# Performance work log

Hardware: AMD Instinct MI355X
Metric: run time of the kernel (lower is better)

## Reference

```python
import jax, jax.numpy as jnp
import numpy as np

N = 50000      # nodes
E = 1200000    # edges (before self loops)
IN = 128       # in_channels
HID = 32       # hidden_channels
HEADS = 2
HC = HID * HEADS  # 64, per-layer output channels
OUT = 40       # classes
NEG_SLOPE = 0.2
BN_EPS = 1e-5


def setup_inputs() -> dict:
    key = jax.random.key(0)
    ks = jax.random.split(key, 20)
    def nrm(k, shape, scale=0.1):
        return jax.random.normal(k, shape, dtype=jnp.float32) * scale
    return {
        "x": jax.random.normal(ks[0], (N, IN), dtype=jnp.float32),
        "edge_index": jax.random.randint(ks[1], (2, E), 0, N),
        "W1": nrm(ks[2], (IN, HC)),
        "a_src1": nrm(ks[3], (HEADS, HID)),
        "a_dst1": nrm(ks[4], (HEADS, HID)),
        "b1": nrm(ks[5], (HC,)),
        "bn_gamma": 1.0 + nrm(ks[6], (HC,)),
        "bn_beta": nrm(ks[7], (HC,)),
        "bn_mean": nrm(ks[8], (HC,)),
        "bn_var": jax.random.uniform(ks[9], (HC,), minval=0.5, maxval=1.5),
        "W2": nrm(ks[10], (HC, HC)),
        "a_src2": nrm(ks[11], (HEADS, HID)),
        "a_dst2": nrm(ks[12], (HEADS, HID)),
        "b2": nrm(ks[13], (HC,)),
        "Wf": nrm(ks[14], (HC, OUT)),
        "bf": nrm(ks[15], (OUT,)),
    }


def _gat_conv(x, src, dst, W, a_s, a_d, b):
    # x: [N, F_in] -> h: [N, H, C]
    h = (x @ W).reshape(N, HEADS, HID)
    alpha_src = jnp.einsum("nhc,hc->nh", h, a_s)  # [N, H]
    alpha_dst = jnp.einsum("nhc,hc->nh", h, a_d)  # [N, H]
    e = alpha_src[src] + alpha_dst[dst]            # [E, H]
    e = jnp.where(e > 0, e, NEG_SLOPE * e)         # leaky_relu(0.2)
    # scatter softmax over edges grouped by dst node
    m = jax.ops.segment_max(e, dst, num_segments=N)
    m = jnp.where(jnp.isfinite(m), m, 0.0)         # isolated nodes -> -inf fill
    ee = jnp.exp(e - m[dst])
    denom = jax.ops.segment_sum(ee, dst, num_segments=N)
    alpha = ee / (denom[dst] + 1e-16)              # [E, H]
    # gather src features, weight by attention, scatter-add to dst
    out = jax.ops.segment_sum(h[src] * alpha[:, :, None], dst, num_segments=N)
    return out.reshape(N, HC) + b                  # concat heads + bias


def reference(x, edge_index, W1, a_src1, a_dst1, b1, bn_gamma, bn_beta,
              bn_mean, bn_var, W2, a_src2, a_dst2, b2, Wf, bf):
    # PyG GATConv adds self loops by default
    loop = jnp.arange(N, dtype=edge_index.dtype)
    src = jnp.concatenate([edge_index[0], loop])
    dst = jnp.concatenate([edge_index[1], loop])

    x1 = _gat_conv(x, src, dst, W1, a_src1, a_dst1, b1)
    x1 = (x1 - bn_mean) / jnp.sqrt(bn_var + BN_EPS) * bn_gamma + bn_beta  # BN eval
    x1 = jax.nn.elu(x1)
    # dropout is identity in eval mode
    x2 = _gat_conv(x1, src, dst, W2, a_src2, a_dst2, b2)
    jk = jnp.maximum(x1, x2)  # JumpingKnowledge 'max'
    logits = jk @ Wf + bf
    return jax.nn.log_softmax(logits, axis=1)
```

## Files before the change

kernel.cpp:

```cpp
#include <hip/hip_runtime.h>
#include <hip/hip_bf16.h>
#include <math.h>

#define N_NODES 50000
#define E_EDGES 1200000
#define E_TOT   (E_EDGES + N_NODES)
#define NEG_SLOPE 0.2f
#define BN_EPS 1e-5f
#define P_PART 196
#define B1 256
#define NSCAN (P_PART * B1)

__device__ __forceinline__ int rl_i(int v, int l) {
    return __builtin_amdgcn_readlane(v, l);
}
__device__ __forceinline__ float rl_f(float v, int l) {
    return __uint_as_float(__builtin_amdgcn_readlane(__float_as_uint(v), l));
}
__device__ __forceinline__ unsigned bf16_bits(float f) {
    unsigned u = __float_as_uint(f);
    return (u + 0x7FFFu + ((u >> 16) & 1u)) >> 16;
}

__global__ void hist_kernel(const int* __restrict__ edst, unsigned* __restrict__ Ghist) {
    __shared__ unsigned hist[P_PART];
    for (int i = threadIdx.x; i < P_PART; i += 256) hist[i] = 0;
    __syncthreads();
    const int chunk = (E_TOT + B1 - 1) / B1;
    const int beg = blockIdx.x * chunk;
    const int end = min(beg + chunk, E_TOT);
    for (int i = beg + threadIdx.x; i < end; i += 256) {
        int d = (i < E_EDGES) ? edst[i] : (i - E_EDGES);
        atomicAdd(&hist[d >> 8], 1u);
    }
    __syncthreads();
    for (int p = threadIdx.x; p < P_PART; p += 256)
        Ghist[p * B1 + blockIdx.x] = hist[p];
}

__global__ void scan2_kernel(const unsigned* __restrict__ Ghist, unsigned* __restrict__ Goff) {
    __shared__ unsigned lds[1024];
    const int t = threadIdx.x;
    const int C = (NSCAN + 1023) / 1024;
    const int beg = t * C;
    const int end = min(beg + C, NSCAN);
    unsigned sum = 0;
    for (int i = beg; i < end; ++i) sum += Ghist[i];
    lds[t] = sum;
    __syncthreads();
    for (int off = 1; off < 1024; off <<= 1) {
        unsigned x = (t >= off) ? lds[t - off] : 0;
        __syncthreads();
        lds[t] += x;
        __syncthreads();
    }
    unsigned run = (t == 0) ? 0 : lds[t - 1];
    for (int i = beg; i < end; ++i) { Goff[i] = run; run += Ghist[i]; }
}

__global__ void partbase_kernel(const unsigned* __restrict__ Goff,
                                int* __restrict__ partbase, int* __restrict__ ptr) {
    int p = threadIdx.x;
    if (p < P_PART) partbase[p] = (int)Goff[p * B1];
    if (p == P_PART) partbase[P_PART] = E_TOT;
    if (p == 0) ptr[N_NODES] = E_TOT;
}

__global__ void scat2_kernel(const int* __restrict__ esrc, const int* __restrict__ edst,
                             const unsigned* __restrict__ Goff, unsigned* __restrict__ Gpart) {
    __shared__ unsigned cur[P_PART];
    for (int p = threadIdx.x; p < P_PART; p += 256) cur[p] = Goff[p * B1 + blockIdx.x];
    __syncthreads();
    const int chunk = (E_TOT + B1 - 1) / B1;
    const int beg = blockIdx.x * chunk;
    const int end = min(beg + chunk, E_TOT);
    for (int i = beg + threadIdx.x; i < end; i += 256) {
        int s = (i < E_EDGES) ? esrc[i] : (i - E_EDGES);
        int d = (i < E_EDGES) ? edst[i] : (i - E_EDGES);
        unsigned slot = atomicAdd(&cur[d >> 8], 1u);
        Gpart[slot] = ((unsigned)(d & 255) << 16) | (unsigned)s;
    }
}

__global__ void csr_kernel(const int* __restrict__ partbase, const unsigned* __restrict__ Gpart,
                           int* __restrict__ ptr, unsigned short* __restrict__ csr,
                           unsigned short* __restrict__ dl16) {
    __shared__ unsigned deg[256];
    __shared__ unsigned scn[256];
    const int p = blockIdx.x;
    const int t = threadIdx.x;
    const int base = partbase[p];
    const int cnt = partbase[p + 1] - base;
    deg[t] = 0;
    __syncthreads();
    for (int i = t; i < cnt; i += 256)
        atomicAdd(&deg[Gpart[base + i] >> 16], 1u);
    __syncthreads();
    unsigned v = deg[t];
    scn[t] = v;
    __syncthreads();
    for (int o = 1; o < 256; o <<= 1) {
        unsigned x = (t >= o) ? scn[t - o] : 0;
        __syncthreads();
        scn[t] += x;
        __syncthreads();
    }
    unsigned excl = scn[t] - v;
    int node = p * 256 + t;
    if (node < N_NODES) ptr[node] = base + (int)excl;
    __syncthreads();
    deg[t] = excl;
    __syncthreads();
    for (int i = t; i < cnt; i += 256) {
        unsigned rec = Gpart[base + i];
        unsigned dl = rec >> 16;
        unsigned slot = atomicAdd(&deg[dl], 1u);
        csr[base + slot]  = (unsigned short)(rec & 0xFFFFu);
        dl16[base + slot] = (unsigned short)dl;
    }
}

__global__ void ew_kernel(const int* __restrict__ partbase,
                          const unsigned short* __restrict__ csr,
                          const unsigned short* __restrict__ dl16,
                          const float2* __restrict__ asrc,
                          const float2* __restrict__ adst,
                          uint2* __restrict__ wrec,
                          float2* __restrict__ denom) {
    __shared__ float2 sad[256];
    __shared__ float sden[512];
    const int p = blockIdx.x, t = threadIdx.x;
    if (t < 256) {
        int node = p * 256 + t;
        sad[t] = (node < N_NODES) ? adst[node] : make_float2(0.f, 0.f);
    }
    if (t < 512) sden[t] = 0.f;
    __syncthreads();
    const int base = partbase[p];
    const int cnt = partbase[p + 1] - base;
    for (int i = t; i < cnt; i += 1024) {
        int s  = (int)csr[base + i];
        int dl = (int)dl16[base + i];
        float2 a = asrc[s];
        float2 b = sad[dl];
        float e0 = a.x + b.x; e0 = e0 > 0.f ? e0 : NEG_SLOPE * e0;
        float e1 = a.y + b.y; e1 = e1 > 0.f ? e1 : NEG_SLOPE * e1;
        float w0 = __expf(e0), w1 = __expf(e1);
        atomicAdd(&sden[dl * 2 + 0], w0);
        atomicAdd(&sden[dl * 2 + 1], w1);
        wrec[base + i] = make_uint2((unsigned)s | (bf16_bits(w0) << 16), bf16_bits(w1));
    }
    __syncthreads();
    if (t < 256) {
        int node = p * 256 + t;
        if (node < N_NODES) denom[node] = make_float2(sden[t * 2], sden[t * 2 + 1]);
    }
}

template<int K>
__global__ __launch_bounds__(256) void lin_att_kernel(
        const float* __restrict__ x, const float* __restrict__ W,
        const float* __restrict__ a_s, const float* __restrict__ a_d,
        __hip_bfloat16* __restrict__ h, float* __restrict__ asrc,
        float* __restrict__ adst) {
    __shared__ float sx[64 * (K + 1)];
    __shared__ float sW[K * 64];
    const int tid = threadIdx.x;
    for (int i = tid; i < K * 64; i += 256) sW[i] = W[i];
    const int ng = tid >> 4;
    const int cg = tid & 15;
    const int c0 = cg * 4;
    const float4 asv = *(const float4*)&a_s[c0];
    const float4 adv = *(const float4*)&a_d[c0];
    const int ntiles = (N_NODES + 63) / 64;
    for (int tile = blockIdx.x; tile < ntiles; tile += gridDim.x) {
        const int nbase = tile * 64;
        __syncthreads();
        for (int i = tid; i < 64 * K; i += 256) {
            int n = i / K, k = i - n * K;
            int node = nbase + n;
            sx[n * (K + 1) + k] = (node < N_NODES) ? x[(size_t)node * K + k] : 0.f;
        }
        __syncthreads();
        float acc[4][4] = {};
        #pragma unroll 4
        for (int k = 0; k < K; ++k) {
            float4 wv = *(const float4*)&sW[k * 64 + c0];
            #pragma unroll
            for (int j = 0; j < 4; ++j) {
                float xv = sx[(ng * 4 + j) * (K + 1) + k];
                acc[j][0] = fmaf(xv, wv.x, acc[j][0]);
                acc[j][1] = fmaf(xv, wv.y, acc[j][1]);
                acc[j][2] = fmaf(xv, wv.z, acc[j][2]);
                acc[j][3] = fmaf(xv, wv.w, acc[j][3]);
            }
        }
        #pragma unroll
        for (int j = 0; j < 4; ++j) {
            int node = nbase + ng * 4 + j;
            float ps = acc[j][0] * asv.x + acc[j][1] * asv.y +
                       acc[j][2] * asv.z + acc[j][3] * asv.w;
            float pd = acc[j][0] * adv.x + acc[j][1] * adv.y +
                       acc[j][2] * adv.z + acc[j][3] * adv.w;
            #pragma unroll
            for (int o = 1; o < 8; o <<= 1) {
                ps += __shfl_xor(ps, o, 64);
                pd += __shfl_xor(pd, o, 64);
            }
            if (node < N_NODES) {
                ushort4 pk;
                pk.x = (unsigned short)bf16_bits(acc[j][0]);
                pk.y = (unsigned short)bf16_bits(acc[j][1]);
                pk.z = (unsigned short)bf16_bits(acc[j][2]);
                pk.w = (unsigned short)bf16_bits(acc[j][3]);
                *(ushort4*)&h[(size_t)node * 64 + c0] = pk;
                if ((cg & 7) == 0) {
                    int head = cg >> 3;
                    asrc[node * 2 + head] = ps;
                    adst[node * 2 + head] = pd;
                }
            }
        }
    }
}

template<bool BN, bool FINAL>
__global__ void gat_agg_kernel(const int* __restrict__ ptr,
                               const uint2* __restrict__ wrec,
                               const float2* __restrict__ denom,
                               const __hip_bfloat16* __restrict__ h,
                               const float* __restrict__ bias,
                               const float* __restrict__ gamma, const float* __restrict__ beta,
                               const float* __restrict__ mean, const float* __restrict__ var,
                               float* __restrict__ out,
                               const float* __restrict__ x1, const float* __restrict__ Wf,
                               const float* __restrict__ bf, float* __restrict__ out40) {
    __shared__ float sWf[FINAL ? 64 * 40 : 1];
    if constexpr (FINAL) {
        for (int i = threadIdx.x; i < 64 * 40; i += 256) sWf[i] = Wf[i];
        __syncthreads();
    }
    int node = blockIdx.x * 4 + (threadIdx.x >> 6);
    if (node >= N_NODES) return;
    const int lane = threadIdx.x & 63;
    const int half = lane & 31;
    const bool lo = (lane < 32);
    float2 dn = denom[node];
    const float den = lo ? dn.x : dn.y;
    float acc = 0.f;
    const int beg = ptr[node], end = ptr[node + 1];

#define EDGE(J) {                                                            \
        unsigned rx = (unsigned)rl_i((int)rec.x, (J));                       \
        unsigned ry = (unsigned)rl_i((int)rec.y, (J));                       \
        const __hip_bfloat16* hp = h + (size_t)(rx & 0xFFFFu) * 64u;         \
        float wv = __uint_as_float(lo ? (rx & 0xFFFF0000u) : (ry << 16));    \
        acc = fmaf(wv, __bfloat162float(hp[lane]), acc); }

    for (int base = beg; base < end; base += 32) {
        const int cnt = min(32, end - base);
        uint2 rec = make_uint2(0u, 0u);
        if (half < cnt) rec = wrec[base + half];
        int j = 0;
        for (; j + 8 <= cnt; j += 8) {
            EDGE(j) EDGE(j + 1) EDGE(j + 2) EDGE(j + 3)
            EDGE(j + 4) EDGE(j + 5) EDGE(j + 6) EDGE(j + 7)
        }
        for (; j < cnt; ++j) { EDGE(j) }
    }
#undef EDGE

    float v = acc / (den + 1e-16f) + bias[lane];
    if constexpr (BN) {
        v = (v - mean[lane]) * rsqrtf(var[lane] + BN_EPS) * gamma[lane] + beta[lane];
        v = v > 0.f ? v : (__expf(v) - 1.f);
    }
    if constexpr (FINAL) {
        float jk = fmaxf(x1[node * 64 + lane], v);
        const int o = (lane < 40) ? lane : 0;
        float dot = 0.f;
        #pragma unroll
        for (int c = 0; c < 64; ++c) {
            float jv = rl_f(jk, c);
            dot = fmaf(jv, sWf[c * 40 + o], dot);
        }
        float logit = (lane < 40) ? (dot + bf[o]) : -INFINITY;
        float mx = logit;
        #pragma unroll
        for (int mm = 1; mm < 64; mm <<= 1) mx = fmaxf(mx, __shfl_xor(mx, mm, 64));
        float ex = (lane < 40) ? __expf(logit - mx) : 0.f;
        float sum = ex;
        #pragma unroll
        for (int mm = 1; mm < 64; mm <<= 1) sum += __shfl_xor(sum, mm, 64);
        if (lane < 40) out40[node * 40 + lane] = logit - mx - logf(sum);
    } else {
        out[node * 64 + lane] = v;
    }
}

extern "C" void kernel_launch(void* const* d_in, const int* in_sizes, int n_in,
                              void* d_out, int out_size, void* d_ws, size_t ws_size,
                              hipStream_t stream) {
    const float* x     = (const float*)d_in[0];
    const int*   ei    = (const int*)d_in[1];
    const float* W1    = (const float*)d_in[2];
    const float* as1   = (const float*)d_in[3];
    const float* ad1   = (const float*)d_in[4];
    const float* b1    = (const float*)d_in[5];
    const float* gamma = (const float*)d_in[6];
    const float* beta  = (const float*)d_in[7];
    const float* mean  = (const float*)d_in[8];
    const float* var   = (const float*)d_in[9];
    const float* W2    = (const float*)d_in[10];
    const float* as2   = (const float*)d_in[11];
    const float* ad2   = (const float*)d_in[12];
    const float* b2    = (const float*)d_in[13];
    const float* Wf    = (const float*)d_in[14];
    const float* bf    = (const float*)d_in[15];
    float* out = (float*)d_out;
    const int* esrc = ei;
    const int* edst = ei + E_EDGES;

    char* ws = (char*)d_ws;
    size_t off = 0;
    auto alloc = [&](size_t bytes) {
        char* p = ws + off;
        off += (bytes + 255) & ~(size_t)255;
        return p;
    };
    unsigned* Ghist = (unsigned*)alloc((size_t)NSCAN * 4);
    unsigned* Goff  = (unsigned*)alloc((size_t)NSCAN * 4);
    int* partbase   = (int*)alloc((size_t)(P_PART + 1) * 4);
    unsigned* Gpart = (unsigned*)alloc((size_t)E_TOT * 4);
    int* ptr              = (int*)alloc((size_t)(N_NODES + 1) * 4);
    unsigned short* csr   = (unsigned short*)alloc((size_t)E_TOT * 2);
    unsigned short* dl16  = (unsigned short*)alloc((size_t)E_TOT * 2);
    uint2* wrec           = (uint2*)alloc((size_t)E_TOT * 8);
    float2* denom         = (float2*)alloc((size_t)N_NODES * 8);
    __hip_bfloat16* hbuf  = (__hip_bfloat16*)alloc((size_t)N_NODES * 64 * 2);
    float* x1buf = (float*)alloc((size_t)N_NODES * 64 * 4);
    float* asrc  = (float*)alloc((size_t)N_NODES * 2 * 4);
    float* adst  = (float*)alloc((size_t)N_NODES * 2 * 4);
    (void)ws_size; (void)in_sizes; (void)n_in; (void)out_size;

    const int NB = (N_NODES + 3) / 4;
    const int GT = (N_NODES + 63) / 64;

    hist_kernel<<<B1, 256, 0, stream>>>(edst, Ghist);
    scan2_kernel<<<1, 1024, 0, stream>>>(Ghist, Goff);
    partbase_kernel<<<1, 256, 0, stream>>>(Goff, partbase, ptr);
    scat2_kernel<<<B1, 256, 0, stream>>>(esrc, edst, Goff, Gpart);
    csr_kernel<<<P_PART, 256, 0, stream>>>(partbase, Gpart, ptr, csr, dl16);

    lin_att_kernel<128><<<GT, 256, 0, stream>>>(x, W1, as1, ad1, hbuf, asrc, adst);
    ew_kernel<<<P_PART, 1024, 0, stream>>>(partbase, csr, dl16,
        (const float2*)asrc, (const float2*)adst, wrec, denom);
    gat_agg_kernel<true, false><<<NB, 256, 0, stream>>>(ptr, wrec, denom, hbuf,
        b1, gamma, beta, mean, var, x1buf, nullptr, nullptr, nullptr, nullptr);

    lin_att_kernel<64><<<GT, 256, 0, stream>>>(x1buf, W2, as2, ad2, hbuf, asrc, adst);
    ew_kernel<<<P_PART, 1024, 0, stream>>>(partbase, csr, dl16,
        (const float2*)asrc, (const float2*)adst, wrec, denom);
    gat_agg_kernel<false, true><<<NB, 256, 0, stream>>>(ptr, wrec, denom, hbuf,
        b2, nullptr, nullptr, nullptr, nullptr, nullptr, x1buf, Wf, bf, out);
}
```

Measured before the change: 269.4 us.

## Move softmax denominator into aggregation, pack CSR records, resize partition kernels

The per-node softmax denominator is no longer built with shared-memory atomics in the edge-weight kernel. Each aggregation wave now sums the bf16 weights itself while it gathers features. The two ushort CSR arrays are merged into one packed 32-bit record array. The edge-weight kernel is split into four 256-thread blocks per partition, and the histogram/scatter block count drops from 256 to 64. This removes atomics, a denom buffer and a synchronisation step, but the denominator is now summed from bf16-rounded weights, which slightly changes the numerics.

```diff
diff --git a/kernel.cpp b/kernel.cpp
--- a/kernel.cpp
+++ b/kernel.cpp
@@ -8,7 +8,7 @@
 #define NEG_SLOPE 0.2f
 #define BN_EPS 1e-5f
 #define P_PART 196
-#define B1 256
+#define B1 64
 #define NSCAN (P_PART * B1)
 
 __device__ __forceinline__ int rl_i(int v, int l) {
@@ -83,8 +83,7 @@
 }
 
 __global__ void csr_kernel(const int* __restrict__ partbase, const unsigned* __restrict__ Gpart,
-                           int* __restrict__ ptr, unsigned short* __restrict__ csr,
-                           unsigned short* __restrict__ dl16) {
+                           int* __restrict__ ptr, unsigned* __restrict__ srec) {
     __shared__ unsigned deg[256];
     __shared__ unsigned scn[256];
     const int p = blockIdx.x;
@@ -113,47 +112,38 @@
     __syncthreads();
     for (int i = t; i < cnt; i += 256) {
         unsigned rec = Gpart[base + i];
-        unsigned dl = rec >> 16;
-        unsigned slot = atomicAdd(&deg[dl], 1u);
-        csr[base + slot]  = (unsigned short)(rec & 0xFFFFu);
-        dl16[base + slot] = (unsigned short)dl;
+        unsigned slot = atomicAdd(&deg[rec >> 16], 1u);
+        srec[base + slot] = rec;
     }
 }
 
 __global__ void ew_kernel(const int* __restrict__ partbase,
-                          const unsigned short* __restrict__ csr,
-                          const unsigned short* __restrict__ dl16,
+                          const unsigned* __restrict__ srec,
                           const float2* __restrict__ asrc,
                           const float2* __restrict__ adst,
-                          uint2* __restrict__ wrec,
-                          float2* __restrict__ denom) {
+                          uint2* __restrict__ wrec) {
     __shared__ float2 sad[256];
-    __shared__ float sden[512];
-    const int p = blockIdx.x, t = threadIdx.x;
-    if (t < 256) {
+    const int p = blockIdx.x >> 2, q = blockIdx.x & 3;
+    const int t = threadIdx.x;
+    {
         int node = p * 256 + t;
         sad[t] = (node < N_NODES) ? adst[node] : make_float2(0.f, 0.f);
     }
-    if (t < 512) sden[t] = 0.f;
     __syncthreads();
     const int base = partbase[p];
     const int cnt = partbase[p + 1] - base;
-    for (int i = t; i < cnt; i += 1024) {
-        int s  = (int)csr[base + i];
-        int dl = (int)dl16[base + i];
+    const int qbeg = base + (cnt * q) / 4;
+    const int qend = base + (cnt * (q + 1)) / 4;
+    for (int i = qbeg + t; i < qend; i += 256) {
+        unsigned rec = srec[i];
+        int s  = (int)(rec & 0xFFFFu);
+        int dl = (int)(rec >> 16);
         float2 a = asrc[s];
         float2 b = sad[dl];
         float e0 = a.x + b.x; e0 = e0 > 0.f ? e0 : NEG_SLOPE * e0;
         float e1 = a.y + b.y; e1 = e1 > 0.f ? e1 : NEG_SLOPE * e1;
-        float w0 = __expf(e0), w1 = __expf(e1);
-        atomicAdd(&sden[dl * 2 + 0], w0);
-        atomicAdd(&sden[dl * 2 + 1], w1);
-        wrec[base + i] = make_uint2((unsigned)s | (bf16_bits(w0) << 16), bf16_bits(w1));
-    }
-    __syncthreads();
-    if (t < 256) {
-        int node = p * 256 + t;
-        if (node < N_NODES) denom[node] = make_float2(sden[t * 2], sden[t * 2 + 1]);
+        wrec[i] = make_uint2((unsigned)s,
+                             bf16_bits(__expf(e0)) | (bf16_bits(__expf(e1)) << 16));
     }
 }
 
@@ -227,7 +217,6 @@
 template<bool BN, bool FINAL>
 __global__ void gat_agg_kernel(const int* __restrict__ ptr,
                                const uint2* __restrict__ wrec,
-                               const float2* __restrict__ denom,
                                const __hip_bfloat16* __restrict__ h,
                                const float* __restrict__ bias,
                                const float* __restrict__ gamma, const float* __restrict__ beta,
@@ -244,18 +233,17 @@
     if (node >= N_NODES) return;
     const int lane = threadIdx.x & 63;
     const int half = lane & 31;
-    const bool lo = (lane < 32);
-    float2 dn = denom[node];
-    const float den = lo ? dn.x : dn.y;
-    float acc = 0.f;
+    const unsigned shl = (lane < 32) ? 16u : 0u;
+    float acc = 0.f, s = 0.f;
     const int beg = ptr[node], end = ptr[node + 1];
 
 #define EDGE(J) {                                                            \
         unsigned rx = (unsigned)rl_i((int)rec.x, (J));                       \
         unsigned ry = (unsigned)rl_i((int)rec.y, (J));                       \
-        const __hip_bfloat16* hp = h + (size_t)(rx & 0xFFFFu) * 64u;         \
-        float wv = __uint_as_float(lo ? (rx & 0xFFFF0000u) : (ry << 16));    \
-        acc = fmaf(wv, __bfloat162float(hp[lane]), acc); }
+        const __hip_bfloat16* hp = h + (size_t)rx * 64u;                     \
+        float wv = __uint_as_float((ry << shl) & 0xFFFF0000u);               \
+        acc = fmaf(wv, __bfloat162float(hp[lane]), acc);                     \
+        s += wv; }
 
     for (int base = beg; base < end; base += 32) {
         const int cnt = min(32, end - base);
@@ -270,7 +258,7 @@
     }
 #undef EDGE
 
-    float v = acc / (den + 1e-16f) + bias[lane];
+    float v = acc / (s + 1e-16f) + bias[lane];
     if constexpr (BN) {
         v = (v - mean[lane]) * rsqrtf(var[lane] + BN_EPS) * gamma[lane] + beta[lane];
         v = v > 0.f ? v : (__expf(v) - 1.f);
@@ -333,10 +321,8 @@
     int* partbase   = (int*)alloc((size_t)(P_PART + 1) * 4);
     unsigned* Gpart = (unsigned*)alloc((size_t)E_TOT * 4);
     int* ptr              = (int*)alloc((size_t)(N_NODES + 1) * 4);
-    unsigned short* csr   = (unsigned short*)alloc((size_t)E_TOT * 2);
-    unsigned short* dl16  = (unsigned short*)alloc((size_t)E_TOT * 2);
+    unsigned* srec        = (unsigned*)alloc((size_t)E_TOT * 4);
     uint2* wrec           = (uint2*)alloc((size_t)E_TOT * 8);
-    float2* denom         = (float2*)alloc((size_t)N_NODES * 8);
     __hip_bfloat16* hbuf  = (__hip_bfloat16*)alloc((size_t)N_NODES * 64 * 2);
     float* x1buf = (float*)alloc((size_t)N_NODES * 64 * 4);
     float* asrc  = (float*)alloc((size_t)N_NODES * 2 * 4);
@@ -350,17 +336,17 @@
     scan2_kernel<<<1, 1024, 0, stream>>>(Ghist, Goff);
     partbase_kernel<<<1, 256, 0, stream>>>(Goff, partbase, ptr);
     scat2_kernel<<<B1, 256, 0, stream>>>(esrc, edst, Goff, Gpart);
-    csr_kernel<<<P_PART, 256, 0, stream>>>(partbase, Gpart, ptr, csr, dl16);
+    csr_kernel<<<P_PART, 256, 0, stream>>>(partbase, Gpart, ptr, srec);
 
     lin_att_kernel<128><<<GT, 256, 0, stream>>>(x, W1, as1, ad1, hbuf, asrc, adst);
-    ew_kernel<<<P_PART, 1024, 0, stream>>>(partbase, csr, dl16,
-        (const float2*)asrc, (const float2*)adst, wrec, denom);
-    gat_agg_kernel<true, false><<<NB, 256, 0, stream>>>(ptr, wrec, denom, hbuf,
+    ew_kernel<<<P_PART * 4, 256, 0, stream>>>(partbase, srec,
+        (const float2*)asrc, (const float2*)adst, wrec);
+    gat_agg_kernel<true, false><<<NB, 256, 0, stream>>>(ptr, wrec, hbuf,
         b1, gamma, beta, mean, var, x1buf, nullptr, nullptr, nullptr, nullptr);
 
     lin_att_kernel<64><<<GT, 256, 0, stream>>>(x1buf, W2, as2, ad2, hbuf, asrc, adst);
-    ew_kernel<<<P_PART, 1024, 0, stream>>>(partbase, csr, dl16,
-        (const float2*)asrc, (const float2*)adst, wrec, denom);
-    gat_agg_kernel<false, true><<<NB, 256, 0, stream>>>(ptr, wrec, denom, hbuf,
+    ew_kernel<<<P_PART * 4, 256, 0, stream>>>(partbase, srec,
+        (const float2*)asrc, (const float2*)adst, wrec);
+    gat_agg_kernel<false, true><<<NB, 256, 0, stream>>>(ptr, wrec, hbuf,
         b2, nullptr, nullptr, nullptr, nullptr, nullptr, x1buf, Wf, bf, out);
 }
```

Result: faster. 261.0 us (-3.1%).
